# Kernel optimization log

Hardware: AMD Instinct MI355X
Metric: run time of the kernel (lower is better)

Reference implementation:

```python
import jax, jax.numpy as jnp
import numpy as np

B, L, D = 4096, 200, 128


def setup_inputs() -> dict:
    key = jax.random.key(0)
    ks = jax.random.split(key, 9)
    s_in = 1.0 / np.sqrt(2 * D)  # torch Linear default init scale (uniform bound)
    inp = {
        "h_states": jax.random.normal(ks[0], (B, L, D), dtype=jnp.float32),
        "target_emb_proj": jax.random.normal(ks[1], (B, D), dtype=jnp.float32),
        "mask": jax.random.randint(ks[2], (B, L), 0, 2).astype(bool),
        "W_r": jax.random.uniform(ks[3], (2 * D, D), jnp.float32, -s_in, s_in),
        "b_r": jax.random.uniform(ks[4], (D,), jnp.float32, -s_in, s_in),
        "W_u": jax.random.uniform(ks[5], (2 * D, D), jnp.float32, -s_in, s_in),
        "b_u": jax.random.uniform(ks[6], (D,), jnp.float32, -s_in, s_in),
        "W_h": jax.random.uniform(ks[7], (2 * D, D), jnp.float32, -s_in, s_in),
        "b_h": jax.random.uniform(ks[8], (D,), jnp.float32, -s_in, s_in),
    }
    return inp


def reference(h_states, target_emb_proj, mask, W_r, b_r, W_u, b_u, W_h, b_h):
    Bd, Ld, Dd = h_states.shape
    # target-aware attention scores over history: (B, L)
    scores = jnp.einsum("bld,bd->bl", h_states, target_emb_proj) / np.sqrt(Dd).astype(h_states.dtype)
    scores = jnp.where(mask, scores, jnp.asarray(-1e9, scores.dtype))
    attn = jax.nn.softmax(scores, axis=-1)  # (B, L)

    xs = (
        jnp.transpose(h_states, (1, 0, 2)),  # (L, B, D)
        attn.T,                               # (L, B)
        mask.T,                               # (L, B)
    )

    def step(h, x):
        x_t, e_t, m_t = x
        combined = jnp.concatenate([x_t, h], axis=-1)  # (B, 2D)
        r = jax.nn.sigmoid(combined @ W_r + b_r)
        u = jax.nn.sigmoid(combined @ W_u + b_u)
        u_prime = e_t[:, None] * u
        h_tilde = jnp.tanh(jnp.concatenate([x_t, r * h], axis=-1) @ W_h + b_h)
        h_new = (1.0 - u_prime) * h + u_prime * h_tilde
        h_next = jnp.where(m_t[:, None], h_new, h)
        return h_next, None

    h0 = jnp.zeros((Bd, Dd), dtype=h_states.dtype)
    h_final, _ = jax.lax.scan(step, h0, xs)
    return h_final
```

## Files before the change

### kernel.cpp

```cpp
#include <hip/hip_runtime.h>
#include <hip/hip_bf16.h>
#include <stdint.h>

#define LSEQ 200
#define DDIM 128

typedef __attribute__((ext_vector_type(8))) __bf16 bf16x8;
typedef __attribute__((ext_vector_type(4))) float f32x4;

__device__ __forceinline__ float fast_exp(float x) {
  return __builtin_amdgcn_exp2f(x * 1.4426950408889634f);
}
__device__ __forceinline__ float fast_sigmoid(float x) {
  return __builtin_amdgcn_rcpf(1.0f + fast_exp(-x));
}
__device__ __forceinline__ float fast_tanh(float x) {
  float ax = __builtin_fabsf(x);
  float t = __builtin_amdgcn_exp2f(ax * -2.885390081777927f);
  float r = (1.0f - t) * __builtin_amdgcn_rcpf(1.0f + t);
  return x < 0.0f ? -r : r;
}
__device__ __forceinline__ f32x4 mfma16(bf16x8 a, bf16x8 b, f32x4 c) {
  return __builtin_amdgcn_mfma_f32_16x16x32_bf16(a, b, c, 0, 0, 0);
}

__global__ __launch_bounds__(512) void k_scores(
    const float* __restrict__ h_states, const float* __restrict__ target,
    const int* __restrict__ mask, uint4* __restrict__ xp,
    float* __restrict__ attnT, int B) {
  __shared__ float s_sc[4][16][LSEQ];
  __shared__ float s_tgt[16][DDIM];
  const int b16 = blockIdx.x;
  const int bb = b16 * 16;
  const int tid = threadIdx.x;
  for (int i = tid; i < 16 * DDIM; i += 512)
    s_tgt[i >> 7][i & 127] = target[(size_t)(bb + (i >> 7)) * DDIM + (i & 127)];
  __syncthreads();

  {
    const int lane = tid & 63;
    const int kt = (tid >> 6) & 3;
    const int tp = tid >> 8;
    const int row = lane & 15;
    const int hi = lane >> 4;
    const int kbase = kt * 32 + hi * 8;
    const float* src = h_states + ((size_t)(bb + row) * LSEQ) * DDIM + kbase;
    const float* tg = &s_tgt[row][kbase];
#pragma unroll 2
    for (int t = tp; t < LSEQ; t += 2) {
      float4 a = *(const float4*)(src + (size_t)t * DDIM);
      float4 b = *(const float4*)(src + (size_t)t * DDIM + 4);
      float dv = (a.x * tg[0] + a.y * tg[1] + a.z * tg[2] + a.w * tg[3]) +
                 (b.x * tg[4] + b.y * tg[5] + b.z * tg[6] + b.w * tg[7]);
      dv += __shfl_xor(dv, 16);
      dv += __shfl_xor(dv, 32);
      if (hi == 0) s_sc[kt][row][t] = dv;
      union { __bf16 h[8]; uint4 v; } pk;
      pk.h[0] = (__bf16)a.x; pk.h[1] = (__bf16)a.y; pk.h[2] = (__bf16)a.z; pk.h[3] = (__bf16)a.w;
      pk.h[4] = (__bf16)b.x; pk.h[5] = (__bf16)b.y; pk.h[6] = (__bf16)b.z; pk.h[7] = (__bf16)b.w;
      xp[(((size_t)b16 * LSEQ + t) * 4 + kt) * 64 + lane] = pk.v;
    }
  }
  __syncthreads();

  if (tid < 256) {
    const int r2 = tid >> 4;
    const int j = tid & 15;
    const int* mrow = mask + (size_t)(bb + r2) * LSEQ;
    float mx = -3.0e38f;
    for (int t = j; t < LSEQ; t += 16) {
      float s = (s_sc[0][r2][t] + s_sc[1][r2][t]) + (s_sc[2][r2][t] + s_sc[3][r2][t]);
      s *= 0.088388347648318447f;
      s = (mrow[t] != 0) ? s : -3.0e38f;
      s_sc[0][r2][t] = s;
      mx = fmaxf(mx, s);
    }
    mx = fmaxf(mx, __shfl_xor(mx, 1));
    mx = fmaxf(mx, __shfl_xor(mx, 2));
    mx = fmaxf(mx, __shfl_xor(mx, 4));
    mx = fmaxf(mx, __shfl_xor(mx, 8));
    float se = 0.0f;
    for (int t = j; t < LSEQ; t += 16) {
      float e = fast_exp(s_sc[0][r2][t] - mx);
      s_sc[1][r2][t] = e;
      se += e;
    }
    se += __shfl_xor(se, 1);
    se += __shfl_xor(se, 2);
    se += __shfl_xor(se, 4);
    se += __shfl_xor(se, 8);
    float rs = __builtin_amdgcn_rcpf(se);
    for (int t = j; t < LSEQ; t += 16)
      attnT[((size_t)b16 * LSEQ + t) * 16 + r2] =
          (mrow[t] != 0) ? s_sc[1][r2][t] * rs : 0.0f;
  }
}

#define STEP(t, XC, XN, AXRC, AXUC, AXHC, AXRN, AXUN, AXHN)                  \
  do {                                                                       \
    if ((t) + 2 < LSEQ) {                                                    \
      _Pragma("unroll") for (int kt = 0; kt < 4; ++kt)                       \
          XN[kt] = xpb[((size_t)(t) + 2) * 256 + kt * 64];                   \
    }                                                                        \
    f32x4 att4 = *(const f32x4*)&s_att[(t)][g * 4];                          \
    bf16x8 hf[4];                                                            \
    _Pragma("unroll") for (int kt = 0; kt < 4; ++kt)                         \
        hf[kt] = __builtin_bit_cast(bf16x8, s_hb_f[kt][lane]);               \
    f32x4 accr = AXRC, accu = AXUC;                                          \
    if ((t) + 1 < LSEQ) {         \
      AXRN = (f32x4){biasr, biasr, biasr, biasr};                            \
      AXUN = (f32x4){biasu, biasu, biasu, biasu};                            \
      _Pragma("unroll") for (int kt = 0; kt < 4; ++kt) {                     \
        bf16x8 a = __builtin_bit_cast(bf16x8, XC[kt]);                       \
        AXRN = mfma16(a, wr[kt], AXRN);                                      \
        AXUN = mfma16(a, wu[kt], AXUN);                                      \
      }                                                                      \
    }                                                                        \
    _Pragma("unroll") for (int kt = 0; kt < 4; ++kt) {                       \
      accr = mfma16(hf[kt], wr[4 + kt], accr);                               \
      accu = mfma16(hf[kt], wu[4 + kt], accu);                               \
    }                                                                        \
    float rr[4], uu[4];                                                      \
    _Pragma("unroll") for (int j = 0; j < 4; ++j) {                          \
      rr[j] = fast_sigmoid(accr[j]);                                         \
      uu[j] = fast_sigmoid(accu[j]);                                         \
      rh_w[j * 8] = (__bf16)(rr[j] * hD[j]);                                 \
    }                                                                        \
    __builtin_amdgcn_sched_barrier(0);                                       \
    asm volatile("s_waitcnt lgkmcnt(0)" ::: "memory");                       \
    __builtin_amdgcn_s_barrier();                                            \
    __builtin_amdgcn_sched_barrier(0);                                       \
    bf16x8 rf[4];                                                            \
    _Pragma("unroll") for (int kt = 0; kt < 4; ++kt)                         \
        rf[kt] = __builtin_bit_cast(bf16x8, s_rh_f[kt][lane]);               \
    f32x4 acch = AXHC;                                                       \
    if ((t) + 1 < LSEQ) {                                                    \
      AXHN = (f32x4){biash, biash, biash, biash};                            \
      _Pragma("unroll") for (int kt = 0; kt < 4; ++kt)                       \
          AXHN = mfma16(__builtin_bit_cast(bf16x8, XC[kt]), wh[kt], AXHN);   \
    }                                                                        \
    _Pragma("unroll") for (int kt = 0; kt < 4; ++kt)                         \
        acch = mfma16(rf[kt], wh[4 + kt], acch);                             \
    _Pragma("unroll") for (int j = 0; j < 4; ++j) {                          \
      float ht = fast_tanh(acch[j]);                                         \
      float up = att4[j] * uu[j];                                            \
      hD[j] += up * (ht - hD[j]);                                            \
      hb_w[j * 8] = (__bf16)hD[j];                                           \
    }                                                                        \
    __builtin_amdgcn_sched_barrier(0);                                       \
    asm volatile("s_waitcnt lgkmcnt(0)" ::: "memory");                       \
    __builtin_amdgcn_s_barrier();                                            \
    __builtin_amdgcn_sched_barrier(0);                                       \
  } while (0)

__global__ __launch_bounds__(512, 2) void k_recur(
    const uint4* __restrict__ xp, const float* __restrict__ attnT,
    const float* __restrict__ Wr, const float* __restrict__ br,
    const float* __restrict__ Wu, const float* __restrict__ bu,
    const float* __restrict__ Wh, const float* __restrict__ bh,
    float* __restrict__ out, int B) {
  __shared__ uint4 s_hb_f[4][64];
  __shared__ uint4 s_rh_f[4][64];
  __shared__ float s_att[LSEQ][16];
  const int tid = threadIdx.x;
  const int lane = tid & 63;
  const int wv = tid >> 6;
  const int b16 = blockIdx.x;
  const int bb = b16 * 16;
  const int g = lane >> 4;
  const int rA = lane & 15;
  const int col = wv * 16 + rA;

  bf16x8 wr[8], wu[8], wh[8];
#pragma unroll
  for (int kt = 0; kt < 8; ++kt) {
    bf16x8 tr, tu, th;
    int krow = kt * 32 + g * 8;
#pragma unroll
    for (int j = 0; j < 8; ++j) {
      tr[j] = (__bf16)Wr[(size_t)(krow + j) * DDIM + col];
      tu[j] = (__bf16)Wu[(size_t)(krow + j) * DDIM + col];
      th[j] = (__bf16)Wh[(size_t)(krow + j) * DDIM + col];
    }
    wr[kt] = tr; wu[kt] = tu; wh[kt] = th;
  }
  const float biasr = br[col], biasu = bu[col], biash = bh[col];

  for (int i = tid; i < LSEQ * 16; i += 512)
    s_att[i >> 4][i & 15] = attnT[(size_t)b16 * LSEQ * 16 + i];
  if (tid < 256) s_hb_f[0][tid & 255] = (uint4){0, 0, 0, 0};

  const int hi_w = (wv & 1) * 2 + (rA >> 3);
  const int e_w = rA & 7;
  __bf16* hb_w = (__bf16*)s_hb_f + (wv >> 1) * 512 + hi_w * 128 + g * 32 + e_w;
  __bf16* rh_w = (__bf16*)s_rh_f + (wv >> 1) * 512 + hi_w * 128 + g * 32 + e_w;

  const uint4* xpb = xp + (size_t)b16 * LSEQ * 256 + lane;

  uint4 xT[4], xA[4], xB[4];
#pragma unroll
  for (int kt = 0; kt < 4; ++kt) xT[kt] = xpb[kt * 64];
#pragma unroll
  for (int kt = 0; kt < 4; ++kt) xA[kt] = xpb[256 + kt * 64];
  f32x4 axr0 = {biasr, biasr, biasr, biasr};
  f32x4 axu0 = {biasu, biasu, biasu, biasu};
  f32x4 axh0 = {biash, biash, biash, biash};
#pragma unroll
  for (int kt = 0; kt < 4; ++kt) {
    bf16x8 a = __builtin_bit_cast(bf16x8, xT[kt]);
    axr0 = mfma16(a, wr[kt], axr0);
    axu0 = mfma16(a, wu[kt], axu0);
    axh0 = mfma16(a, wh[kt], axh0);
  }
  f32x4 axr1, axu1, axh1;
  float hD[4] = {0.f, 0.f, 0.f, 0.f};
  __syncthreads();

  for (int t = 0; t < LSEQ; t += 2) {
    STEP(t, xA, xB, axr0, axu0, axh0, axr1, axu1, axh1);
    STEP(t + 1, xB, xA, axr1, axu1, axh1, axr0, axu0, axh0);
  }

#pragma unroll
  for (int j = 0; j < 4; ++j)
    out[(size_t)(bb + g * 4 + j) * DDIM + col] = hD[j];
}

extern "C" void kernel_launch(void* const* d_in, const int* in_sizes, int n_in,
                              void* d_out, int out_size, void* d_ws, size_t ws_size,
                              hipStream_t stream) {
  const float* h_states = (const float*)d_in[0];
  const float* target   = (const float*)d_in[1];
  const int*   mask     = (const int*)d_in[2];
  const float* Wr = (const float*)d_in[3];
  const float* br = (const float*)d_in[4];
  const float* Wu = (const float*)d_in[5];
  const float* bu = (const float*)d_in[6];
  const float* Wh = (const float*)d_in[7];
  const float* bh = (const float*)d_in[8];

  const int B = in_sizes[0] / (LSEQ * DDIM);
  uint4* xp = (uint4*)d_ws;
  float* attnT = (float*)((char*)d_ws + (size_t)B * LSEQ * DDIM * 2);

  k_scores<<<B / 16, 512, 0, stream>>>(h_states, target, mask, xp, attnT, B);
  k_recur<<<B / 16, 512, 0, stream>>>(xp, attnT, Wr, br, Wu, bu, Wh, bh,
                                      (float*)d_out, B);
}
```

Baseline: 347.4 us.

## Transpose MFMA operands, vectorize LDS writes, and split the recurrent accumulation chains

Swaps the A and B operands of every MFMA so each lane's accumulator holds four consecutive hidden columns for one batch row. The bf16 h and r*h values can then be written to LDS as one 8-byte store per lane instead of four scalar stores, and the final output becomes a float4 store. The recurrent-part MFMAs are split into two independent accumulator chains that are summed at the end, which shortens the serial MFMA dependency on the critical path. Two sched_barriers are also removed, and the attention weight becomes a single scalar read per lane.

```diff
diff --git a/kernel.cpp b/kernel.cpp
--- a/kernel.cpp
+++ b/kernel.cpp
@@ -102,52 +102,59 @@
       _Pragma("unroll") for (int kt = 0; kt < 4; ++kt)                       \
           XN[kt] = xpb[((size_t)(t) + 2) * 256 + kt * 64];                   \
     }                                                                        \
-    f32x4 att4 = *(const f32x4*)&s_att[(t)][g * 4];                          \
+    float att = s_att[(t)][rA];                                              \
     bf16x8 hf[4];                                                            \
     _Pragma("unroll") for (int kt = 0; kt < 4; ++kt)                         \
         hf[kt] = __builtin_bit_cast(bf16x8, s_hb_f[kt][lane]);               \
-    f32x4 accr = AXRC, accu = AXUC;                                          \
     if ((t) + 1 < LSEQ) {         \
-      AXRN = (f32x4){biasr, biasr, biasr, biasr};                            \
-      AXUN = (f32x4){biasu, biasu, biasu, biasu};                            \
+      AXRN = vbr;                                                            \
+      AXUN = vbu;                                                            \
       _Pragma("unroll") for (int kt = 0; kt < 4; ++kt) {                     \
-        bf16x8 a = __builtin_bit_cast(bf16x8, XC[kt]);                       \
-        AXRN = mfma16(a, wr[kt], AXRN);                                      \
-        AXUN = mfma16(a, wu[kt], AXUN);                                      \
+        bf16x8 b = __builtin_bit_cast(bf16x8, XC[kt]);                       \
+        AXRN = mfma16(wr[kt], b, AXRN);                                      \
+        AXUN = mfma16(wu[kt], b, AXUN);                                      \
       }                                                                      \
     }                                                                        \
-    _Pragma("unroll") for (int kt = 0; kt < 4; ++kt) {                       \
-      accr = mfma16(hf[kt], wr[4 + kt], accr);                               \
-      accu = mfma16(hf[kt], wu[4 + kt], accu);                               \
-    }                                                                        \
+    f32x4 r1 = AXRC, u1 = AXUC;                                              \
+    f32x4 r2 = {0.f, 0.f, 0.f, 0.f}, u2 = {0.f, 0.f, 0.f, 0.f};              \
+    r1 = mfma16(wr[4], hf[0], r1); u1 = mfma16(wu[4], hf[0], u1);            \
+    r2 = mfma16(wr[6], hf[2], r2); u2 = mfma16(wu[6], hf[2], u2);            \
+    r1 = mfma16(wr[5], hf[1], r1); u1 = mfma16(wu[5], hf[1], u1);            \
+    r2 = mfma16(wr[7], hf[3], r2); u2 = mfma16(wu[7], hf[3], u2);            \
+    f32x4 accr = r1 + r2, accu = u1 + u2;                                    \
     float rr[4], uu[4];                                                      \
+    union { __bf16 h[4]; uint2 v; } rhv;                                     \
     _Pragma("unroll") for (int j = 0; j < 4; ++j) {                          \
       rr[j] = fast_sigmoid(accr[j]);                                         \
       uu[j] = fast_sigmoid(accu[j]);                                         \
-      rh_w[j * 8] = (__bf16)(rr[j] * hD[j]);                                 \
-    }                                                                        \
-    __builtin_amdgcn_sched_barrier(0);                                       \
+      rhv.h[j] = (__bf16)(rr[j] * hD[j]);                                    \
+    }                                                                        \
+    *rh_w = rhv.v;                                                           \
     asm volatile("s_waitcnt lgkmcnt(0)" ::: "memory");                       \
     __builtin_amdgcn_s_barrier();                                            \
     __builtin_amdgcn_sched_barrier(0);                                       \
     bf16x8 rf[4];                                                            \
     _Pragma("unroll") for (int kt = 0; kt < 4; ++kt)                         \
         rf[kt] = __builtin_bit_cast(bf16x8, s_rh_f[kt][lane]);               \
-    f32x4 acch = AXHC;                                                       \
     if ((t) + 1 < LSEQ) {                                                    \
-      AXHN = (f32x4){biash, biash, biash, biash};                            \
+      AXHN = vbh;                                                            \
       _Pragma("unroll") for (int kt = 0; kt < 4; ++kt)                       \
-          AXHN = mfma16(__builtin_bit_cast(bf16x8, XC[kt]), wh[kt], AXHN);   \
-    }                                                                        \
-    _Pragma("unroll") for (int kt = 0; kt < 4; ++kt)                         \
-        acch = mfma16(rf[kt], wh[4 + kt], acch);                             \
+          AXHN = mfma16(wh[kt], __builtin_bit_cast(bf16x8, XC[kt]), AXHN);   \
+    }                                                                        \
+    f32x4 h1 = AXHC, h2 = {0.f, 0.f, 0.f, 0.f};                              \
+    h1 = mfma16(wh[4], rf[0], h1);                                           \
+    h2 = mfma16(wh[6], rf[2], h2);                                           \
+    h1 = mfma16(wh[5], rf[1], h1);                                           \
+    h2 = mfma16(wh[7], rf[3], h2);                                           \
+    f32x4 acch = h1 + h2;                                                    \
+    union { __bf16 h[4]; uint2 v; } hbv;                                     \
     _Pragma("unroll") for (int j = 0; j < 4; ++j) {                          \
       float ht = fast_tanh(acch[j]);                                         \
-      float up = att4[j] * uu[j];                                            \
+      float up = att * uu[j];                                                \
       hD[j] += up * (ht - hD[j]);                                            \
-      hb_w[j * 8] = (__bf16)hD[j];                                           \
-    }                                                                        \
-    __builtin_amdgcn_sched_barrier(0);                                       \
+      hbv.h[j] = (__bf16)hD[j];                                              \
+    }                                                                        \
+    *hb_w = hbv.v;                                                           \
     asm volatile("s_waitcnt lgkmcnt(0)" ::: "memory");                       \
     __builtin_amdgcn_s_barrier();                                            \
     __builtin_amdgcn_sched_barrier(0);                                       \
@@ -167,7 +174,7 @@
   const int wv = tid >> 6;
   const int b16 = blockIdx.x;
   const int bb = b16 * 16;
-  const int g = lane >> 4;
+  const int q = lane >> 4;
   const int rA = lane & 15;
   const int col = wv * 16 + rA;
 
@@ -175,7 +182,7 @@
 #pragma unroll
   for (int kt = 0; kt < 8; ++kt) {
     bf16x8 tr, tu, th;
-    int krow = kt * 32 + g * 8;
+    int krow = kt * 32 + q * 8;
 #pragma unroll
     for (int j = 0; j < 8; ++j) {
       tr[j] = (__bf16)Wr[(size_t)(krow + j) * DDIM + col];
@@ -184,16 +191,18 @@
     }
     wr[kt] = tr; wu[kt] = tu; wh[kt] = th;
   }
-  const float biasr = br[col], biasu = bu[col], biash = bh[col];
+  const int cbase = wv * 16 + q * 4;
+  f32x4 vbr = {br[cbase], br[cbase + 1], br[cbase + 2], br[cbase + 3]};
+  f32x4 vbu = {bu[cbase], bu[cbase + 1], bu[cbase + 2], bu[cbase + 3]};
+  f32x4 vbh = {bh[cbase], bh[cbase + 1], bh[cbase + 2], bh[cbase + 3]};
 
   for (int i = tid; i < LSEQ * 16; i += 512)
     s_att[i >> 4][i & 15] = attnT[(size_t)b16 * LSEQ * 16 + i];
   if (tid < 256) s_hb_f[0][tid & 255] = (uint4){0, 0, 0, 0};
 
-  const int hi_w = (wv & 1) * 2 + (rA >> 3);
-  const int e_w = rA & 7;
-  __bf16* hb_w = (__bf16*)s_hb_f + (wv >> 1) * 512 + hi_w * 128 + g * 32 + e_w;
-  __bf16* rh_w = (__bf16*)s_rh_f + (wv >> 1) * 512 + hi_w * 128 + g * 32 + e_w;
+  const int lane_w = rA + 16 * ((wv & 1) * 2 + (q >> 1));
+  uint2* hb_w = (uint2*)((char*)s_hb_f + (wv >> 1) * 1024 + lane_w * 16 + (q & 1) * 8);
+  uint2* rh_w = (uint2*)((char*)s_rh_f + (wv >> 1) * 1024 + lane_w * 16 + (q & 1) * 8);
 
   const uint4* xpb = xp + (size_t)b16 * LSEQ * 256 + lane;
 
@@ -202,15 +211,13 @@
   for (int kt = 0; kt < 4; ++kt) xT[kt] = xpb[kt * 64];
 #pragma unroll
   for (int kt = 0; kt < 4; ++kt) xA[kt] = xpb[256 + kt * 64];
-  f32x4 axr0 = {biasr, biasr, biasr, biasr};
-  f32x4 axu0 = {biasu, biasu, biasu, biasu};
-  f32x4 axh0 = {biash, biash, biash, biash};
+  f32x4 axr0 = vbr, axu0 = vbu, axh0 = vbh;
 #pragma unroll
   for (int kt = 0; kt < 4; ++kt) {
-    bf16x8 a = __builtin_bit_cast(bf16x8, xT[kt]);
-    axr0 = mfma16(a, wr[kt], axr0);
-    axu0 = mfma16(a, wu[kt], axu0);
-    axh0 = mfma16(a, wh[kt], axh0);
+    bf16x8 b = __builtin_bit_cast(bf16x8, xT[kt]);
+    axr0 = mfma16(wr[kt], b, axr0);
+    axu0 = mfma16(wu[kt], b, axu0);
+    axh0 = mfma16(wh[kt], b, axh0);
   }
   f32x4 axr1, axu1, axh1;
   float hD[4] = {0.f, 0.f, 0.f, 0.f};
@@ -221,9 +228,8 @@
     STEP(t + 1, xB, xA, axr1, axu1, axh1, axr0, axu0, axh0);
   }
 
-#pragma unroll
-  for (int j = 0; j < 4; ++j)
-    out[(size_t)(bb + g * 4 + j) * DDIM + col] = hD[j];
+  float4 o = {hD[0], hD[1], hD[2], hD[3]};
+  *(float4*)(out + (size_t)(bb + rA) * DDIM + cbase) = o;
 }
 
 extern "C" void kernel_launch(void* const* d_in, const int* in_sizes, int n_in,
```

After: 341.5 us. About the same (-1.7%).
